# Performance work log

Measured on AMD Instinct MI355X. Metric: run time of the kernel, lower is better.

The kernel has to match this reference:

```python
import jax, jax.numpy as jnp
import numpy as np

VOCAB, E, U, T, B = 32000, 256, 512, 512, 128

def setup_inputs() -> dict:
    key = jax.random.key(0)
    ks = jax.random.split(key, 12)
    s = lambda k, shape, scale: jax.random.normal(k, shape, dtype=jnp.float32) * scale
    return {
        "sentence": jax.random.randint(ks[0], (B, T), 0, VOCAB, dtype=jnp.int32),
        "emb": s(ks[1], (VOCAB, E), 0.05),
        "Wx": s(ks[2], (E, 4 * U), 1.0 / np.sqrt(E)),   # input->gates (i,f,g,o)
        "Wh": s(ks[3], (U, 4 * U), 1.0 / np.sqrt(U)),   # hidden->gates
        "b":  jnp.zeros((4 * U,), dtype=jnp.float32),
        "W1": s(ks[4], (U, 128), 1.0 / np.sqrt(U)),
        "b1": jnp.zeros((128,), dtype=jnp.float32),
        "W2": s(ks[5], (128, 64), 1.0 / np.sqrt(128)),
        "b2": jnp.zeros((64,), dtype=jnp.float32),
        "W3": s(ks[6], (64, 1), 1.0 / np.sqrt(64)),
        "b3": jnp.zeros((1,), dtype=jnp.float32),
    }

def reference(sentence, emb, Wx, Wh, b, W1, b1, W2, b2, W3, b3):
    # Embedding lookup: [B, T, E]
    x = emb[sentence]
    batch = x.shape[0]
    units = Wh.shape[0]
    h0 = jnp.zeros((batch, units), dtype=x.dtype)
    c0 = jnp.zeros((batch, units), dtype=x.dtype)

    def step(carry, xt):
        h, c = carry
        z = xt @ Wx + h @ Wh + b                      # [B, 4U]
        i, f, g, o = jnp.split(z, 4, axis=-1)
        i = jax.nn.sigmoid(i)
        f = jax.nn.sigmoid(f)
        g = jnp.tanh(g)
        o = jax.nn.sigmoid(o)
        c_new = f * c + i * g
        h_new = o * jnp.tanh(c_new)
        return (h_new, c_new), None

    (h, _), _ = jax.lax.scan(step, (h0, c0), jnp.swapaxes(x, 0, 1))  # scan over T
    h1 = jax.nn.relu(h @ W1 + b1)
    h2 = jax.nn.relu(h1 @ W2 + b2)
    return jax.nn.sigmoid(h2 @ W3 + b3)               # [B, 1]
```

## Files before the change

### kernel.cpp

```cpp
#include <hip/hip_runtime.h>
#include <hip/hip_bf16.h>
#include <hip/hip_fp16.h>


#define B_ 128
#define T_ 512
#define E_ 256
#define U_ 512
#define NWG_ 128
#define HROW_ 516

typedef __attribute__((ext_vector_type(4))) _Float16 half4;
typedef __attribute__((ext_vector_type(4))) float floatx4;
typedef unsigned long long u64t;
typedef unsigned int u32t;

#define MFMA16 __builtin_amdgcn_mfma_f32_16x16x16f16

__device__ __forceinline__ float sigmf(float x) { return 1.0f / (1.0f + __expf(-x)); }
__device__ __forceinline__ float tanh_f(float x) { return 2.0f / (1.0f + __expf(-2.0f * x)) - 1.0f; }

__global__ void prep_x_kernel(const int* __restrict__ sent,
                              const float* __restrict__ emb,
                              _Float16* __restrict__ X) {
  int gid = blockIdx.x * blockDim.x + threadIdx.x;
  int e8 = gid & 31;
  int row = gid >> 5;
  int b = row & 127;
  int t = row >> 7;
  int word = sent[b * T_ + t];
  const float* src = emb + (size_t)word * E_ + e8 * 8;
  float4 v0 = *(const float4*)(src);
  float4 v1 = *(const float4*)(src + 4);
  _Float16 o[8] = {(_Float16)v0.x, (_Float16)v0.y, (_Float16)v0.z, (_Float16)v0.w,
                   (_Float16)v1.x, (_Float16)v1.y, (_Float16)v1.z, (_Float16)v1.w};
  _Float16* dst = X + (size_t)row * E_ + e8 * 8;
  *(half4*)dst = *(half4*)o;
  *(half4*)(dst + 4) = *(half4*)(o + 4);
}

__global__ __launch_bounds__(512, 1) void lstm_kernel(
    const _Float16* __restrict__ X,
    const float* __restrict__ Wx, const float* __restrict__ Wh,
    const float* __restrict__ bias,
    _Float16* __restrict__ Hq, u32t* FlagA, u32t* FlagB, u32t* XccTab) {
  __shared__ __align__(16) char smem[98304];
  _Float16* Hs = (_Float16*)smem;
  float* Rs = (float*)(smem + 16512);
  u32t* xl = (u32t*)(smem + 24704);
  volatile u32t* goP = (volatile u32t*)(smem + 25216);
  u32t* pcntP = (u32t*)(smem + 25220);

  const int bid = blockIdx.x;
  const int d = bid & 7;
  const int s = bid >> 3;
  const int tid = threadIdx.x;
  const int lane = tid & 63;
  const int wave = tid >> 6;
  const int p16 = lane & 15;
  const int quad = lane >> 4;
  const int sg = wave & 3;
  const int kh = wave >> 2;

  if (tid == 0) {
    *goP = 0u;
    *pcntP = 0u;
    u32t myx = (u32t)__builtin_amdgcn_s_getreg(63508) & 0xFFu;
    __hip_atomic_store(XccTab + bid, 0x5A5A0000u | myx, __ATOMIC_RELAXED,
                       __HIP_MEMORY_SCOPE_AGENT);
  }
  if (wave == 0) {
    u32t v0, v1;
    for (;;) {
      v0 = __hip_atomic_load(XccTab + lane, __ATOMIC_RELAXED,
                             __HIP_MEMORY_SCOPE_AGENT);
      v1 = __hip_atomic_load(XccTab + 64 + lane, __ATOMIC_RELAXED,
                             __HIP_MEMORY_SCOPE_AGENT);
      if (__all(((v0 >> 16) == 0x5A5Au) & ((v1 >> 16) == 0x5A5Au))) break;
      __builtin_amdgcn_s_sleep(8);
    }
    xl[lane] = v0;
    xl[lane + 64] = v1;
  }
  __syncthreads();
  int fastv;
  {
    const u32t ref = xl[d];
    bool dom = true;
    for (int j = 1; j < 16; ++j) dom = dom && (xl[d + 8 * j] == ref);
    bool sane = false;
    const u32t z0 = xl[0];
    for (int e = 1; e < 128; ++e) sane = sane || (xl[e] != z0);
    fastv = (dom && sane) ? 1 : 0;
  }
  const bool fastp = (bool)__builtin_amdgcn_readfirstlane(fastv);

  const int C0 = ((p16 >> 3) & 1) * 512 + s * 32 + sg * 8 + (p16 & 7);
  const int C1 = C0 + 1024;
  half4 b0r[32], b1r[32];
  if (kh == 0) {
#pragma unroll
    for (int i = 0; i < 16; ++i) {
      int kb = 16 + i;
#pragma unroll
      for (int j = 0; j < 4; ++j) {
        int gk = kb * 16 + quad * 4 + j;
        b0r[i][j] = (_Float16)Wh[(size_t)(gk - E_) * 2048 + C0];
        b1r[i][j] = (_Float16)Wh[(size_t)(gk - E_) * 2048 + C1];
      }
    }
  } else {
#pragma unroll
    for (int i = 0; i < 32; ++i) {
      int kb = (i < 16) ? i : (16 + i);
#pragma unroll
      for (int j = 0; j < 4; ++j) {
        int gk = kb * 16 + quad * 4 + j;
        float w0 = (gk < E_) ? Wx[(size_t)gk * 2048 + C0]
                             : Wh[(size_t)(gk - E_) * 2048 + C0];
        float w1 = (gk < E_) ? Wx[(size_t)gk * 2048 + C1]
                             : Wh[(size_t)(gk - E_) * 2048 + C1];
        b0r[i][j] = (_Float16)w0;
        b1r[i][j] = (_Float16)w1;
      }
    }
  }

  const bool lo = (p16 < 8);
  const int uo = p16 & 7;
  const int gu = s * 32 + sg * 8 + uo;
  const float bias0 = bias[(lo ? 0 : 512) + gu];
  const float bias1 = bias[(lo ? 1024 : 1536) + gu];

  float cst[4] = {0.f, 0.f, 0.f, 0.f};

  const int brow = d * 16 + p16;
  const int ko = quad * 4;

  for (int t = 0; t < T_; ++t) {
    const int pin = t & 1, pout = pin ^ 1;

    floatx4 acc0 = {0.f, 0.f, 0.f, 0.f};
    floatx4 acc1 = {0.f, 0.f, 0.f, 0.f};

    u32t gv = (u32t)t;

    if (kh == 1) {
      const _Float16* xr = X + ((size_t)t * B_ + brow) * E_ + ko;
#pragma unroll
      for (int i = 0; i < 16; ++i) {
        half4 a = *(const half4*)(xr + i * 16);
        acc0 = MFMA16(a, b0r[i], acc0, 0, 0, 0);
        acc1 = MFMA16(a, b1r[i], acc1, 0, 0, 0);
      }
    } else if (t > 0) {
      const u32t tgt = (u32t)t;
      if (wave == 0) {
        u32t v;
        if (fastp) {
          u32t* fa = FlagA + (size_t)(pin * 8 + d) * 16;
          const u32t* fb = FlagB + (size_t)(pin * 8 + d) * 16;
          int budget = 6;
          for (;;) {
            if (budget > 0) {
              u32t old = tgt;
              if (lane < 16) {
                u32t* ap = fa + lane;
                asm volatile(
                    "global_atomic_add %0, %1, %2, off sc0\n\t"
                    "s_waitcnt vmcnt(0)"
                    : "=&v"(old) : "v"(ap), "v"(0u) : "memory");
              }
              v = old;
            } else {
              v = (lane < 16)
                      ? __hip_atomic_load(fb + lane, __ATOMIC_RELAXED,
                                          __HIP_MEMORY_SCOPE_AGENT)
                      : tgt;
            }
            if (__all(v == tgt)) break;
            --budget;
            if (budget < 4) __builtin_amdgcn_s_sleep(1);
          }
        } else {
          const u32t* fb = FlagB + (size_t)(pin * 8 + d) * 16;
          for (;;) {
            v = (lane < 16)
                    ? __hip_atomic_load(fb + lane, __ATOMIC_RELAXED,
                                        __HIP_MEMORY_SCOPE_AGENT)
                    : tgt;
            if (__all(v == tgt)) break;
            __builtin_amdgcn_s_sleep(1);
          }
        }
        gv = v;
        if (lane == 0) *goP = tgt;
      } else {
        u32t g;
        do { g = *goP; } while (g < tgt);
        gv = g;
      }
      const size_t dep = (size_t)(gv >> 16);

      const _Float16* hq =
          Hq + ((size_t)(pin * 8 + d) * 16 + wave * 4) * 512 + dep;
      u64t hv[8];
      if (fastp) {
        const u64t* hqb = (const u64t*)hq + lane;
        u64t h0, h1, h2, h3, h4, h5, h6, h7;
        asm volatile(
            "global_load_dwordx2 %0, %8, off sc0\n\t"
            "global_load_dwordx2 %1, %8, off offset:512 sc0\n\t"
            "global_load_dwordx2 %2, %8, off offset:1024 sc0\n\t"
            "global_load_dwordx2 %3, %8, off offset:1536 sc0\n\t"
            "global_load_dwordx2 %4, %8, off offset:2048 sc0\n\t"
            "global_load_dwordx2 %5, %8, off offset:2560 sc0\n\t"
            "global_load_dwordx2 %6, %8, off offset:3072 sc0\n\t"
            "global_load_dwordx2 %7, %8, off offset:3584 sc0\n\t"
            "s_waitcnt vmcnt(0)"
            : "=&v"(h0), "=&v"(h1), "=&v"(h2), "=&v"(h3),
              "=&v"(h4), "=&v"(h5), "=&v"(h6), "=&v"(h7)
            : "v"(hqb)
            : "memory");
        hv[0] = h0; hv[1] = h1; hv[2] = h2; hv[3] = h3;
        hv[4] = h4; hv[5] = h5; hv[6] = h6; hv[7] = h7;
      } else {
#pragma unroll
        for (int j = 0; j < 8; ++j) {
          size_t idx = (size_t)(j >> 1) * 128 + (j & 1) * 64 + lane;
          hv[j] = __hip_atomic_load((const u64t*)hq + idx, __ATOMIC_RELAXED,
                                    __HIP_MEMORY_SCOPE_AGENT);
        }
      }
#pragma unroll
      for (int j = 0; j < 8; ++j) {
        int r = wave * 4 + (j >> 1), half = j & 1;
        *(u64t*)(Hs + r * HROW_ + half * 256 + lane * 4) = hv[j];
      }
    }
    __syncthreads();

    if (t > 0) {
#pragma unroll
      for (int i = 0; i < 16; ++i) {
        int hk = kh * 16 + i;
        half4 a = *(const half4*)(Hs + p16 * HROW_ + hk * 16 + ko);
        const int wi = (kh == 0) ? i : (16 + i);
        acc0 = MFMA16(a, b0r[wi], acc0, 0, 0, 0);
        acc1 = MFMA16(a, b1r[wi], acc1, 0, 0, 0);
      }
    }

    if (kh == 1) {
      float* wb = Rs + sg * 512;
      *(floatx4*)(wb + lane * 4) = acc0;
      *(floatx4*)(wb + 256 + lane * 4) = acc1;
    }
    __syncthreads();

    if (kh == 0) {
      const float* rb = Rs + sg * 512;
      floatx4 z0v = acc0 + *(const floatx4*)(rb + lane * 4);
      floatx4 z1v = acc1 + *(const floatx4*)(rb + 256 + lane * 4);
#pragma unroll
      for (int r = 0; r < 4; ++r) {
        float z0 = z0v[r] + bias0;
        float z1 = z1v[r] + bias1;
        float s0 = sigmf(z0);
        float s1 = lo ? tanh_f(z1) : sigmf(z1);
        float prod = s0 * s1;
        float fg = __shfl_xor(lo ? prod : s0, 8, 64);
        float og = __shfl_xor(s1, 8, 64);
        if (lo) {
          float cn = fg * cst[r] + prod;
          cst[r] = cn;
          float h = og * tanh_f(cn);
          int rowl = quad * 4 + r;
          _Float16 hf16 = (_Float16)h;
          unsigned short hb = __builtin_bit_cast(unsigned short, hf16);
          unsigned short* hp =
              (unsigned short*)(Hq +
                                ((size_t)(pout * 8 + d) * 16 + rowl) * 512 + gu);
          if (fastp) {
            *hp = hb;
          } else {
            __hip_atomic_store(hp, hb, __ATOMIC_RELAXED,
                               __HIP_MEMORY_SCOPE_AGENT);
          }
        }
      }

      asm volatile("s_waitcnt vmcnt(0)" ::: "memory");
      __builtin_amdgcn_sched_barrier(0);
      if (lane == 0) {
        u32t old = atomicAdd(pcntP, 1u);
        if (old == (u32t)(4 * t + 3)) {
          size_t fo = (size_t)(pout * 8 + d) * 16 + s;
          if (fastp) {
            u32t* ap = FlagA + fo;
            u32t nv = (u32t)(t + 1);
            asm volatile("global_atomic_swap %0, %1, off"
                         :: "v"(ap), "v"(nv) : "memory");
          }
          __hip_atomic_store(FlagB + fo, (u32t)(t + 1), __ATOMIC_RELAXED,
                             __HIP_MEMORY_SCOPE_AGENT);
        }
      }
    }
  }
}

__global__ void head_kernel(const _Float16* __restrict__ Hq,
                            const float* __restrict__ W1, const float* __restrict__ b1,
                            const float* __restrict__ W2, const float* __restrict__ b2,
                            const float* __restrict__ W3, const float* __restrict__ b3,
                            float* __restrict__ out) {
  __shared__ float hs[512];
  __shared__ float h1[128];
  __shared__ float h2[64];
  int row = blockIdx.x;
  int tid = threadIdx.x;
  int dd = row >> 4, rr = row & 15;
  const _Float16* hrow = Hq + ((size_t)dd * 16 + rr) * 512;
  for (int k = tid; k < 512; k += 128) hs[k] = (float)hrow[k];
  __syncthreads();
  float a = b1[tid];
  for (int k = 0; k < 512; ++k) a += hs[k] * W1[k * 128 + tid];
  h1[tid] = fmaxf(a, 0.0f);
  __syncthreads();
  if (tid < 64) {
    float a2 = b2[tid];
    for (int k = 0; k < 128; ++k) a2 += h1[k] * W2[k * 64 + tid];
    h2[tid] = fmaxf(a2, 0.0f);
  }
  __syncthreads();
  if (tid == 0) {
    float a3 = b3[0];
    for (int k = 0; k < 64; ++k) a3 += h2[k] * W3[k];
    out[row] = 1.0f / (1.0f + __expf(-a3));
  }
}

extern "C" void kernel_launch(void* const* d_in, const int* in_sizes, int n_in,
                              void* d_out, int out_size, void* d_ws, size_t ws_size,
                              hipStream_t stream) {
  const int* sent = (const int*)d_in[0];
  const float* emb = (const float*)d_in[1];
  const float* Wx = (const float*)d_in[2];
  const float* Wh = (const float*)d_in[3];
  const float* b = (const float*)d_in[4];
  const float* W1 = (const float*)d_in[5];
  const float* b1 = (const float*)d_in[6];
  const float* W2 = (const float*)d_in[7];
  const float* b2 = (const float*)d_in[8];
  const float* W3 = (const float*)d_in[9];
  const float* b3 = (const float*)d_in[10];
  float* out = (float*)d_out;

  char* ws = (char*)d_ws;
  _Float16* X = (_Float16*)(ws);
  _Float16* Hq = (_Float16*)(ws + (size_t)33554432);
  u32t* FlagA = (u32t*)(ws + (size_t)33554432 + 262144);
  u32t* FlagB = (u32t*)(ws + (size_t)33554432 + 263168);
  u32t* XccTab = (u32t*)(ws + (size_t)33554432 + 264192);

  hipMemsetAsync(FlagA, 0, 2560, stream);
  prep_x_kernel<<<8192, 256, 0, stream>>>(sent, emb, X);
  lstm_kernel<<<NWG_, 512, 0, stream>>>(X, Wx, Wh, b, Hq, FlagA, FlagB, XccTab);
  head_kernel<<<128, 128, 0, stream>>>(Hq, W1, b1, W2, b2, W3, b3, out);
}
```

Measured before the change: 1.848 ms.

## Load hidden-state fragments directly into MFMA operands, dropping LDS staging barrier

Each wave now reads its own hidden-state A-operand fragments straight from the global exchange buffer into registers instead of cooperatively staging them into shared memory. This removes the LDS write/read round trip and one __syncthreads per timestep. The reduction buffer is double-buffered by step parity so the remaining barrier suffices. In exchange, every wave issues twice as many small strided global loads, and waves that were previously doing the x-projection now also wait on the go flag and the hidden-state fetch.

```diff
diff --git a/kernel.cpp b/kernel.cpp
--- a/kernel.cpp
+++ b/kernel.cpp
@@ -8,7 +8,6 @@
 #define E_ 256
 #define U_ 512
 #define NWG_ 128
-#define HROW_ 516
 
 typedef __attribute__((ext_vector_type(4))) _Float16 half4;
 typedef __attribute__((ext_vector_type(4))) float floatx4;
@@ -45,11 +44,10 @@
     const float* __restrict__ bias,
     _Float16* __restrict__ Hq, u32t* FlagA, u32t* FlagB, u32t* XccTab) {
   __shared__ __align__(16) char smem[98304];
-  _Float16* Hs = (_Float16*)smem;
-  float* Rs = (float*)(smem + 16512);
-  u32t* xl = (u32t*)(smem + 24704);
-  volatile u32t* goP = (volatile u32t*)(smem + 25216);
-  u32t* pcntP = (u32t*)(smem + 25220);
+  float* Rs = (float*)smem;
+  u32t* xl = (u32t*)(smem + 16384);
+  volatile u32t* goP = (volatile u32t*)(smem + 16896);
+  u32t* pcntP = (u32t*)(smem + 16900);
 
   const int bid = blockIdx.x;
   const int d = bid & 7;
@@ -143,8 +141,6 @@
     floatx4 acc0 = {0.f, 0.f, 0.f, 0.f};
     floatx4 acc1 = {0.f, 0.f, 0.f, 0.f};
 
-    u32t gv = (u32t)t;
-
     if (kh == 1) {
       const _Float16* xr = X + ((size_t)t * B_ + brow) * E_ + ko;
 #pragma unroll
@@ -153,8 +149,11 @@
         acc0 = MFMA16(a, b0r[i], acc0, 0, 0, 0);
         acc1 = MFMA16(a, b1r[i], acc1, 0, 0, 0);
       }
-    } else if (t > 0) {
+    }
+
+    if (t > 0) {
       const u32t tgt = (u32t)t;
+      u32t gv;
       if (wave == 0) {
         u32t v;
         if (fastp) {
@@ -202,49 +201,55 @@
       }
       const size_t dep = (size_t)(gv >> 16);
 
-      const _Float16* hq =
-          Hq + ((size_t)(pin * 8 + d) * 16 + wave * 4) * 512 + dep;
-      u64t hv[8];
+      const _Float16* rowp =
+          Hq + ((size_t)(pin * 8 + d) * 16 + p16) * 512 + kh * 256 + quad * 4 +
+          dep;
+      u64t hv[16];
       if (fastp) {
-        const u64t* hqb = (const u64t*)hq + lane;
-        u64t h0, h1, h2, h3, h4, h5, h6, h7;
+        const u64t* gb = (const u64t*)rowp;
+        u64t h0, h1, h2, h3, h4, h5, h6, h7, h8, h9, hA, hB, hC, hD, hE, hF;
         asm volatile(
             "global_load_dwordx2 %0, %8, off sc0\n\t"
-            "global_load_dwordx2 %1, %8, off offset:512 sc0\n\t"
-            "global_load_dwordx2 %2, %8, off offset:1024 sc0\n\t"
-            "global_load_dwordx2 %3, %8, off offset:1536 sc0\n\t"
-            "global_load_dwordx2 %4, %8, off offset:2048 sc0\n\t"
-            "global_load_dwordx2 %5, %8, off offset:2560 sc0\n\t"
-            "global_load_dwordx2 %6, %8, off offset:3072 sc0\n\t"
-            "global_load_dwordx2 %7, %8, off offset:3584 sc0\n\t"
-            "s_waitcnt vmcnt(0)"
+            "global_load_dwordx2 %1, %8, off offset:32 sc0\n\t"
+            "global_load_dwordx2 %2, %8, off offset:64 sc0\n\t"
+            "global_load_dwordx2 %3, %8, off offset:96 sc0\n\t"
+            "global_load_dwordx2 %4, %8, off offset:128 sc0\n\t"
+            "global_load_dwordx2 %5, %8, off offset:160 sc0\n\t"
+            "global_load_dwordx2 %6, %8, off offset:192 sc0\n\t"
+            "global_load_dwordx2 %7, %8, off offset:224 sc0"
             : "=&v"(h0), "=&v"(h1), "=&v"(h2), "=&v"(h3),
               "=&v"(h4), "=&v"(h5), "=&v"(h6), "=&v"(h7)
-            : "v"(hqb)
+            : "v"(gb)
+            : "memory");
+        asm volatile(
+            "global_load_dwordx2 %0, %8, off offset:256 sc0\n\t"
+            "global_load_dwordx2 %1, %8, off offset:288 sc0\n\t"
+            "global_load_dwordx2 %2, %8, off offset:320 sc0\n\t"
+            "global_load_dwordx2 %3, %8, off offset:352 sc0\n\t"
+            "global_load_dwordx2 %4, %8, off offset:384 sc0\n\t"
+            "global_load_dwordx2 %5, %8, off offset:416 sc0\n\t"
+            "global_load_dwordx2 %6, %8, off offset:448 sc0\n\t"
+            "global_load_dwordx2 %7, %8, off offset:480 sc0\n\t"
+            "s_waitcnt vmcnt(0)"
+            : "=&v"(h8), "=&v"(h9), "=&v"(hA), "=&v"(hB),
+              "=&v"(hC), "=&v"(hD), "=&v"(hE), "=&v"(hF)
+            : "v"(gb)
             : "memory");
         hv[0] = h0; hv[1] = h1; hv[2] = h2; hv[3] = h3;
         hv[4] = h4; hv[5] = h5; hv[6] = h6; hv[7] = h7;
+        hv[8] = h8; hv[9] = h9; hv[10] = hA; hv[11] = hB;
+        hv[12] = hC; hv[13] = hD; hv[14] = hE; hv[15] = hF;
       } else {
 #pragma unroll
-        for (int j = 0; j < 8; ++j) {
-          size_t idx = (size_t)(j >> 1) * 128 + (j & 1) * 64 + lane;
-          hv[j] = __hip_atomic_load((const u64t*)hq + idx, __ATOMIC_RELAXED,
+        for (int j = 0; j < 16; ++j) {
+          hv[j] = __hip_atomic_load((const u64t*)rowp + (size_t)j * 4,
+                                    __ATOMIC_RELAXED,
                                     __HIP_MEMORY_SCOPE_AGENT);
         }
       }
 #pragma unroll
-      for (int j = 0; j < 8; ++j) {
-        int r = wave * 4 + (j >> 1), half = j & 1;
-        *(u64t*)(Hs + r * HROW_ + half * 256 + lane * 4) = hv[j];
-      }
-    }
-    __syncthreads();
-
-    if (t > 0) {
-#pragma unroll
       for (int i = 0; i < 16; ++i) {
-        int hk = kh * 16 + i;
-        half4 a = *(const half4*)(Hs + p16 * HROW_ + hk * 16 + ko);
+        half4 a = __builtin_bit_cast(half4, hv[i]);
         const int wi = (kh == 0) ? i : (16 + i);
         acc0 = MFMA16(a, b0r[wi], acc0, 0, 0, 0);
         acc1 = MFMA16(a, b1r[wi], acc1, 0, 0, 0);
@@ -252,14 +257,14 @@
     }
 
     if (kh == 1) {
-      float* wb = Rs + sg * 512;
+      float* wb = Rs + pin * 2048 + sg * 512;
       *(floatx4*)(wb + lane * 4) = acc0;
       *(floatx4*)(wb + 256 + lane * 4) = acc1;
     }
     __syncthreads();
 
     if (kh == 0) {
-      const float* rb = Rs + sg * 512;
+      const float* rb = Rs + pin * 2048 + sg * 512;
       floatx4 z0v = acc0 + *(const floatx4*)(rb + lane * 4);
       floatx4 z1v = acc1 + *(const floatx4*)(rb + 256 + lane * 4);
 #pragma unroll
```

New measurement: 3.314 ms. +79.3%, slower.

## Transpose MFMA operands to pack hidden-state stores and drop dependency trick

Applied to the files above, without the earlier changes.

Swaps the MFMA A/B operands so each lane holds four consecutive units for one batch row. The gate nonlinearities can then be computed with a single xor-32 shuffle pairing, and the new h values are written as one 64-bit packed store instead of four scattered 16-bit stores. The change also removes the fake address dependency derived from the flag value, loads the biases as vectors, and raises the atomic polling budget before the wave starts sleeping. This cuts global store traffic and shuffle work on the serial critical path, but dropping the flag-to-load dependency could allow stale hidden-state reads if ordering was relying on it.

```diff
diff --git a/kernel.cpp b/kernel.cpp
--- a/kernel.cpp
+++ b/kernel.cpp
@@ -126,11 +126,11 @@
     }
   }
 
-  const bool lo = (p16 < 8);
-  const int uo = p16 & 7;
-  const int gu = s * 32 + sg * 8 + uo;
-  const float bias0 = bias[(lo ? 0 : 512) + gu];
-  const float bias1 = bias[(lo ? 1024 : 1536) + gu];
+  const int u0 = s * 32 + sg * 8 + (quad & 1) * 4;
+  const floatx4 bi = *(const floatx4*)(bias + u0);
+  const floatx4 bf = *(const floatx4*)(bias + 512 + u0);
+  const floatx4 bg = *(const floatx4*)(bias + 1024 + u0);
+  const floatx4 bo = *(const floatx4*)(bias + 1536 + u0);
 
   float cst[4] = {0.f, 0.f, 0.f, 0.f};
 
@@ -143,15 +143,13 @@
     floatx4 acc0 = {0.f, 0.f, 0.f, 0.f};
     floatx4 acc1 = {0.f, 0.f, 0.f, 0.f};
 
-    u32t gv = (u32t)t;
-
     if (kh == 1) {
       const _Float16* xr = X + ((size_t)t * B_ + brow) * E_ + ko;
 #pragma unroll
       for (int i = 0; i < 16; ++i) {
         half4 a = *(const half4*)(xr + i * 16);
-        acc0 = MFMA16(a, b0r[i], acc0, 0, 0, 0);
-        acc1 = MFMA16(a, b1r[i], acc1, 0, 0, 0);
+        acc0 = MFMA16(b0r[i], a, acc0, 0, 0, 0);
+        acc1 = MFMA16(b1r[i], a, acc1, 0, 0, 0);
       }
     } else if (t > 0) {
       const u32t tgt = (u32t)t;
@@ -160,7 +158,7 @@
         if (fastp) {
           u32t* fa = FlagA + (size_t)(pin * 8 + d) * 16;
           const u32t* fb = FlagB + (size_t)(pin * 8 + d) * 16;
-          int budget = 6;
+          int budget = 512;
           for (;;) {
             if (budget > 0) {
               u32t old = tgt;
@@ -180,7 +178,7 @@
             }
             if (__all(v == tgt)) break;
             --budget;
-            if (budget < 4) __builtin_amdgcn_s_sleep(1);
+            if (budget < 500) __builtin_amdgcn_s_sleep(1);
           }
         } else {
           const u32t* fb = FlagB + (size_t)(pin * 8 + d) * 16;
@@ -193,17 +191,13 @@
             __builtin_amdgcn_s_sleep(1);
           }
         }
-        gv = v;
         if (lane == 0) *goP = tgt;
       } else {
         u32t g;
         do { g = *goP; } while (g < tgt);
-        gv = g;
-      }
-      const size_t dep = (size_t)(gv >> 16);
-
-      const _Float16* hq =
-          Hq + ((size_t)(pin * 8 + d) * 16 + wave * 4) * 512 + dep;
+      }
+
+      const _Float16* hq = Hq + ((size_t)(pin * 8 + d) * 16 + wave * 4) * 512;
       u64t hv[8];
       if (fastp) {
         const u64t* hqb = (const u64t*)hq + lane;
@@ -246,8 +240,8 @@
         int hk = kh * 16 + i;
         half4 a = *(const half4*)(Hs + p16 * HROW_ + hk * 16 + ko);
         const int wi = (kh == 0) ? i : (16 + i);
-        acc0 = MFMA16(a, b0r[wi], acc0, 0, 0, 0);
-        acc1 = MFMA16(a, b1r[wi], acc1, 0, 0, 0);
+        acc0 = MFMA16(b0r[wi], a, acc0, 0, 0, 0);
+        acc1 = MFMA16(b1r[wi], a, acc1, 0, 0, 0);
       }
     }
 
@@ -262,31 +256,28 @@
       const float* rb = Rs + sg * 512;
       floatx4 z0v = acc0 + *(const floatx4*)(rb + lane * 4);
       floatx4 z1v = acc1 + *(const floatx4*)(rb + 256 + lane * 4);
+      half4 hp4;
 #pragma unroll
       for (int r = 0; r < 4; ++r) {
-        float z0 = z0v[r] + bias0;
-        float z1 = z1v[r] + bias1;
-        float s0 = sigmf(z0);
-        float s1 = lo ? tanh_f(z1) : sigmf(z1);
-        float prod = s0 * s1;
-        float fg = __shfl_xor(lo ? prod : s0, 8, 64);
-        float og = __shfl_xor(s1, 8, 64);
-        if (lo) {
-          float cn = fg * cst[r] + prod;
-          cst[r] = cn;
-          float h = og * tanh_f(cn);
-          int rowl = quad * 4 + r;
-          _Float16 hf16 = (_Float16)h;
-          unsigned short hb = __builtin_bit_cast(unsigned short, hf16);
-          unsigned short* hp =
-              (unsigned short*)(Hq +
-                                ((size_t)(pout * 8 + d) * 16 + rowl) * 512 + gu);
-          if (fastp) {
-            *hp = hb;
-          } else {
-            __hip_atomic_store(hp, hb, __ATOMIC_RELAXED,
-                               __HIP_MEMORY_SCOPE_AGENT);
-          }
+        float fraw = __shfl_xor(z0v[r], 32, 64);
+        float oraw = __shfl_xor(z1v[r], 32, 64);
+        float iv = sigmf(z0v[r] + bi[r]);
+        float gv = tanh_f(z1v[r] + bg[r]);
+        float fv = sigmf(fraw + bf[r]);
+        float ov = sigmf(oraw + bo[r]);
+        float cn = fv * cst[r] + iv * gv;
+        cst[r] = cn;
+        hp4[r] = (_Float16)(ov * tanh_f(cn));
+      }
+      if (quad < 2) {
+        u64t pk = __builtin_bit_cast(u64t, hp4);
+        u64t* hp =
+            (u64t*)(Hq + ((size_t)(pout * 8 + d) * 16 + p16) * 512 + u0);
+        if (fastp) {
+          *hp = pk;
+        } else {
+          __hip_atomic_store(hp, pk, __ATOMIC_RELAXED,
+                             __HIP_MEMORY_SCOPE_AGENT);
         }
       }
 
```

After: 1.776 ms (median of 2 runs). -3.9%, faster.
